# Optimization experiments

Measured on AMD Instinct MI355X. Metric: run time of the kernel, lower is better.

## Reference

```python
import jax, jax.numpy as jnp
import numpy as np

H = 32

def setup_inputs() -> dict:
    key = jax.random.key(0)
    ks = jax.random.split(key, 8)
    B, S = 256, 4096
    scale = 1.0 / np.sqrt(H)
    return {
        "lstm_outputs": jax.random.normal(ks[0], (B, S, H), dtype=jnp.float32),
        "final_hidden": jax.random.normal(ks[1], (B, H), dtype=jnp.float32),
        "Wq": jax.random.uniform(ks[2], (H, H), jnp.float32, -scale, scale),
        "bq": jax.random.uniform(ks[3], (H,), jnp.float32, -scale, scale),
        "Wk": jax.random.uniform(ks[4], (H, H), jnp.float32, -scale, scale),
        "bk": jax.random.uniform(ks[5], (H,), jnp.float32, -scale, scale),
        "Wv": jax.random.uniform(ks[6], (H, 1), jnp.float32, -scale, scale),
        "bv": jax.random.uniform(ks[7], (1,), jnp.float32, -scale, scale),
    }

def reference(lstm_outputs, final_hidden, Wq, bq, Wk, bk, Wv, bv):
    # keys: [B,S,H], query: [B,H]
    keys = jnp.einsum('bsh,hd->bsd', lstm_outputs, Wk) + bk
    query = final_hidden @ Wq + bq
    tanhed = jnp.tanh(query[:, None, :] + keys)            # [B,S,H]
    scores = jnp.einsum('bsh,h->bs', tanhed, Wv[:, 0]) + bv[0]  # [B,S]
    att_weights = jax.nn.softmax(scores, axis=-1)          # [B,S]
    context = jnp.einsum('bs,bsh->bh', att_weights, keys)  # [B,H]
    return context, att_weights
```

## Files before the change

kernel.cpp:

```cpp
#include <hip/hip_runtime.h>
#include <math.h>

#define HD 32
#define BB 256
#define SS 4096
#define CHUNK 512
#define NC (SS / CHUNK)
#define BLK 256
#define PART_STRIDE 34

__device__ __forceinline__ float tanh_fast(float x) {
  float e = __builtin_amdgcn_exp2f(x * 2.8853900817779268f);
  return 1.0f - 2.0f * __builtin_amdgcn_rcpf(e + 1.0f);
}
__device__ __forceinline__ float exp_fast(float x) {
  return __builtin_amdgcn_exp2f(x * 1.4426950408889634f);
}

__global__ void __launch_bounds__(BLK) bahdanau_p1(
    const float* __restrict__ lstm, const float* __restrict__ fh,
    const float* __restrict__ Wq, const float* __restrict__ bq,
    const float* __restrict__ Wk, const float* __restrict__ bk,
    const float* __restrict__ Wv, const float* __restrict__ bv,
    float* __restrict__ scores_out, float* __restrict__ partials) {
  __shared__ float sWk[HD * HD];
  __shared__ float sQ[HD];
  __shared__ float sWv[HD];
  __shared__ float sBk[HD];
  __shared__ float sRedM[BLK / 64];
  __shared__ float sRedL[BLK / 64];
  __shared__ float sRedC[BLK / 64][HD];

  const int tid = threadIdx.x;
  const int b = blockIdx.x / NC;
  const int chunk = blockIdx.x % NC;
  const int base = chunk * CHUNK;

  ((float4*)sWk)[tid] = ((const float4*)Wk)[tid];
  if (tid < HD) {
    sWv[tid] = Wv[tid];
    sBk[tid] = bk[tid];
    float acc = bq[tid];
    const float* fhb = fh + b * HD;
#pragma unroll
    for (int j = 0; j < HD; j++) acc += fhb[j] * Wq[j * HD + tid];
    sQ[tid] = acc;
  }
  __syncthreads();

  const int sA = base + tid;
  const int sB = sA + BLK;
  const float* rowA = lstm + ((size_t)b * SS + sA) * HD;
  const float* rowB = rowA + (size_t)BLK * HD;

  float4 xA[8], xB[8];
#pragma unroll
  for (int q = 0; q < 8; q++) {
    xA[q] = ((const float4*)rowA)[q];
    xB[q] = ((const float4*)rowB)[q];
  }

  float keyA[HD], keyB[HD];
#pragma unroll
  for (int q = 0; q < 8; q++) {
    float4 b4 = ((const float4*)sBk)[q];
    keyA[4 * q + 0] = b4.x; keyA[4 * q + 1] = b4.y;
    keyA[4 * q + 2] = b4.z; keyA[4 * q + 3] = b4.w;
    keyB[4 * q + 0] = b4.x; keyB[4 * q + 1] = b4.y;
    keyB[4 * q + 2] = b4.z; keyB[4 * q + 3] = b4.w;
  }

#pragma unroll
  for (int jq = 0; jq < 8; jq++) {
    const float a4[4] = {xA[jq].x, xA[jq].y, xA[jq].z, xA[jq].w};
    const float c4[4] = {xB[jq].x, xB[jq].y, xB[jq].z, xB[jq].w};
#pragma unroll
    for (int jj = 0; jj < 4; jj++) {
      const float aj = a4[jj];
      const float cj = c4[jj];
      const float* wrow = sWk + (jq * 4 + jj) * HD;
#pragma unroll
      for (int hq = 0; hq < 8; hq++) {
        float4 w = ((const float4*)wrow)[hq];
        keyA[4 * hq + 0] += aj * w.x; keyA[4 * hq + 1] += aj * w.y;
        keyA[4 * hq + 2] += aj * w.z; keyA[4 * hq + 3] += aj * w.w;
        keyB[4 * hq + 0] += cj * w.x; keyB[4 * hq + 1] += cj * w.y;
        keyB[4 * hq + 2] += cj * w.z; keyB[4 * hq + 3] += cj * w.w;
      }
    }
  }

  const float bv0 = bv[0];
  float scA = bv0, scB = bv0;
#pragma unroll
  for (int h = 0; h < HD; h++) {
    const float q = sQ[h], wv = sWv[h];
    scA += tanh_fast(q + keyA[h]) * wv;
    scB += tanh_fast(q + keyB[h]) * wv;
  }
  scores_out[(size_t)b * SS + sA] = scA;
  scores_out[(size_t)b * SS + sB] = scB;

  const int wid = tid >> 6, lane = tid & 63;
  float m = fmaxf(scA, scB);
#pragma unroll
  for (int off = 32; off >= 1; off >>= 1) m = fmaxf(m, __shfl_xor(m, off, 64));
  if (lane == 0) sRedM[wid] = m;
  __syncthreads();
  m = fmaxf(fmaxf(sRedM[0], sRedM[1]), fmaxf(sRedM[2], sRedM[3]));

  const float eA = exp_fast(scA - m);
  const float eB = exp_fast(scB - m);
  float l = eA + eB;
#pragma unroll
  for (int off = 32; off >= 1; off >>= 1) l += __shfl_xor(l, off, 64);
  if (lane == 0) sRedL[wid] = l;

#pragma unroll
  for (int h = 0; h < HD; h++) {
    float v = eA * keyA[h] + eB * keyB[h];
#pragma unroll
    for (int off = 32; off >= 1; off >>= 1) v += __shfl_xor(v, off, 64);
    if (lane == 0) sRedC[wid][h] = v;
  }
  __syncthreads();

  if (tid < HD) {
    float c = sRedC[0][tid] + sRedC[1][tid] + sRedC[2][tid] + sRedC[3][tid];
    float* p = partials + (size_t)(b * NC + chunk) * PART_STRIDE;
    p[2 + tid] = c;
    if (tid == 0) {
      p[0] = m;
      p[1] = sRedL[0] + sRedL[1] + sRedL[2] + sRedL[3];
    }
  }
}

__global__ void __launch_bounds__(BLK) bahdanau_p2(
    const float* __restrict__ partials, float* __restrict__ ctx_out,
    float* __restrict__ scores) {
  const int b = blockIdx.x;
  const int tid = threadIdx.x;
  __shared__ float sM, sInvL;
  __shared__ float sAl[NC];

  if (tid == 0) {
    float m = -1e30f;
    for (int c = 0; c < NC; c++)
      m = fmaxf(m, partials[(size_t)(b * NC + c) * PART_STRIDE]);
    float L = 0.f;
    for (int c = 0; c < NC; c++) {
      const float* p = partials + (size_t)(b * NC + c) * PART_STRIDE;
      float a = exp_fast(p[0] - m);
      sAl[c] = a;
      L += a * p[1];
    }
    sM = m;
    sInvL = __builtin_amdgcn_rcpf(L);
  }
  __syncthreads();
  const float m = sM, invL = sInvL;

  if (tid < HD) {
    float c = 0.f;
#pragma unroll
    for (int cc = 0; cc < NC; cc++)
      c += sAl[cc] * partials[(size_t)(b * NC + cc) * PART_STRIDE + 2 + tid];
    ctx_out[b * HD + tid] = c * invL;
  }

  float* srow = scores + (size_t)b * SS;
  for (int s = tid; s < SS; s += BLK) {
    srow[s] = exp_fast(srow[s] - m) * invL;
  }
}

extern "C" void kernel_launch(void* const* d_in, const int* in_sizes, int n_in,
                              void* d_out, int out_size, void* d_ws,
                              size_t ws_size, hipStream_t stream) {
  const float* lstm = (const float*)d_in[0];
  const float* fh   = (const float*)d_in[1];
  const float* Wq   = (const float*)d_in[2];
  const float* bq   = (const float*)d_in[3];
  const float* Wk   = (const float*)d_in[4];
  const float* bk   = (const float*)d_in[5];
  const float* Wv   = (const float*)d_in[6];
  const float* bv   = (const float*)d_in[7];

  float* out = (float*)d_out;
  float* ctx_out = out;
  float* scores = out + BB * HD;
  float* partials = (float*)d_ws;

  bahdanau_p1<<<BB * NC, BLK, 0, stream>>>(lstm, fh, Wq, bq, Wk, bk, Wv, bv,
                                           scores, partials);
  bahdanau_p2<<<BB, BLK, 0, stream>>>(partials, ctx_out, scores);
}
```

Before: 249.3 us.

## Read Wk via uniform scalar loads, hoist row loads, split normalize kernel per chunk

```diff
diff --git a/kernel.cpp b/kernel.cpp
--- a/kernel.cpp
+++ b/kernel.cpp
@@ -9,6 +9,8 @@
 #define BLK 256
 #define PART_STRIDE 34
 
+typedef float vf32 __attribute__((ext_vector_type(32)));
+
 __device__ __forceinline__ float tanh_fast(float x) {
   float e = __builtin_amdgcn_exp2f(x * 2.8853900817779268f);
   return 1.0f - 2.0f * __builtin_amdgcn_rcpf(e + 1.0f);
@@ -17,16 +19,13 @@
   return __builtin_amdgcn_exp2f(x * 1.4426950408889634f);
 }
 
-__global__ void __launch_bounds__(BLK) bahdanau_p1(
+__global__ void __launch_bounds__(BLK, 3) bahdanau_p1(
     const float* __restrict__ lstm, const float* __restrict__ fh,
     const float* __restrict__ Wq, const float* __restrict__ bq,
     const float* __restrict__ Wk, const float* __restrict__ bk,
     const float* __restrict__ Wv, const float* __restrict__ bv,
     float* __restrict__ scores_out, float* __restrict__ partials) {
-  __shared__ float sWk[HD * HD];
   __shared__ float sQ[HD];
-  __shared__ float sWv[HD];
-  __shared__ float sBk[HD];
   __shared__ float sRedM[BLK / 64];
   __shared__ float sRedL[BLK / 64];
   __shared__ float sRedC[BLK / 64][HD];
@@ -36,10 +35,26 @@
   const int chunk = blockIdx.x % NC;
   const int base = chunk * CHUNK;
 
-  ((float4*)sWk)[tid] = ((const float4*)Wk)[tid];
+  const int sA = base + tid;
+  const int sB = sA + BLK;
+  const float* rowA = lstm + ((size_t)b * SS + sA) * HD;
+  const float* rowB = rowA + (size_t)BLK * HD;
+
+  vf32 xA, xB;
+#pragma unroll
+  for (int q = 0; q < 8; q++) {
+    float4 t = ((const float4*)rowA)[q];
+    xA[4 * q + 0] = t.x; xA[4 * q + 1] = t.y;
+    xA[4 * q + 2] = t.z; xA[4 * q + 3] = t.w;
+  }
+#pragma unroll
+  for (int q = 0; q < 8; q++) {
+    float4 t = ((const float4*)rowB)[q];
+    xB[4 * q + 0] = t.x; xB[4 * q + 1] = t.y;
+    xB[4 * q + 2] = t.z; xB[4 * q + 3] = t.w;
+  }
+
   if (tid < HD) {
-    sWv[tid] = Wv[tid];
-    sBk[tid] = bk[tid];
     float acc = bq[tid];
     const float* fhb = fh + b * HD;
 #pragma unroll
@@ -48,45 +63,21 @@
   }
   __syncthreads();
 
-  const int sA = base + tid;
-  const int sB = sA + BLK;
-  const float* rowA = lstm + ((size_t)b * SS + sA) * HD;
-  const float* rowB = rowA + (size_t)BLK * HD;
-
-  float4 xA[8], xB[8];
+  vf32 kA, kB;
 #pragma unroll
-  for (int q = 0; q < 8; q++) {
-    xA[q] = ((const float4*)rowA)[q];
-    xB[q] = ((const float4*)rowB)[q];
+  for (int h = 0; h < HD; h++) {
+    float bkh = bk[h];
+    kA[h] = bkh; kB[h] = bkh;
   }
-
-  float keyA[HD], keyB[HD];
 #pragma unroll
-  for (int q = 0; q < 8; q++) {
-    float4 b4 = ((const float4*)sBk)[q];
-    keyA[4 * q + 0] = b4.x; keyA[4 * q + 1] = b4.y;
-    keyA[4 * q + 2] = b4.z; keyA[4 * q + 3] = b4.w;
-    keyB[4 * q + 0] = b4.x; keyB[4 * q + 1] = b4.y;
-    keyB[4 * q + 2] = b4.z; keyB[4 * q + 3] = b4.w;
-  }
-
+  for (int j = 0; j < HD; j++) {
+    const float xa = xA[j];
+    const float xb = xB[j];
 #pragma unroll
-  for (int jq = 0; jq < 8; jq++) {
-    const float a4[4] = {xA[jq].x, xA[jq].y, xA[jq].z, xA[jq].w};
-    const float c4[4] = {xB[jq].x, xB[jq].y, xB[jq].z, xB[jq].w};
-#pragma unroll
-    for (int jj = 0; jj < 4; jj++) {
-      const float aj = a4[jj];
-      const float cj = c4[jj];
-      const float* wrow = sWk + (jq * 4 + jj) * HD;
-#pragma unroll
-      for (int hq = 0; hq < 8; hq++) {
-        float4 w = ((const float4*)wrow)[hq];
-        keyA[4 * hq + 0] += aj * w.x; keyA[4 * hq + 1] += aj * w.y;
-        keyA[4 * hq + 2] += aj * w.z; keyA[4 * hq + 3] += aj * w.w;
-        keyB[4 * hq + 0] += cj * w.x; keyB[4 * hq + 1] += cj * w.y;
-        keyB[4 * hq + 2] += cj * w.z; keyB[4 * hq + 3] += cj * w.w;
-      }
+    for (int h = 0; h < HD; h++) {
+      const float w = Wk[j * HD + h];
+      kA[h] = fmaf(xa, w, kA[h]);
+      kB[h] = fmaf(xb, w, kB[h]);
     }
   }
 
@@ -94,9 +85,10 @@
   float scA = bv0, scB = bv0;
 #pragma unroll
   for (int h = 0; h < HD; h++) {
-    const float q = sQ[h], wv = sWv[h];
-    scA += tanh_fast(q + keyA[h]) * wv;
-    scB += tanh_fast(q + keyB[h]) * wv;
+    const float qh = sQ[h];
+    const float wv = Wv[h];
+    scA = fmaf(tanh_fast(qh + kA[h]), wv, scA);
+    scB = fmaf(tanh_fast(qh + kB[h]), wv, scB);
   }
   scores_out[(size_t)b * SS + sA] = scA;
   scores_out[(size_t)b * SS + sB] = scB;
@@ -118,7 +110,7 @@
 
 #pragma unroll
   for (int h = 0; h < HD; h++) {
-    float v = eA * keyA[h] + eB * keyB[h];
+    float v = fmaf(eA, kA[h], eB * kB[h]);
 #pragma unroll
     for (int off = 32; off >= 1; off >>= 1) v += __shfl_xor(v, off, 64);
     if (lane == 0) sRedC[wid][h] = v;
@@ -139,40 +131,38 @@
 __global__ void __launch_bounds__(BLK) bahdanau_p2(
     const float* __restrict__ partials, float* __restrict__ ctx_out,
     float* __restrict__ scores) {
-  const int b = blockIdx.x;
+  const int b = blockIdx.x / NC;
+  const int chunk = blockIdx.x % NC;
   const int tid = threadIdx.x;
-  __shared__ float sM, sInvL;
-  __shared__ float sAl[NC];
 
-  if (tid == 0) {
-    float m = -1e30f;
-    for (int c = 0; c < NC; c++)
-      m = fmaxf(m, partials[(size_t)(b * NC + c) * PART_STRIDE]);
-    float L = 0.f;
-    for (int c = 0; c < NC; c++) {
-      const float* p = partials + (size_t)(b * NC + c) * PART_STRIDE;
-      float a = exp_fast(p[0] - m);
-      sAl[c] = a;
-      L += a * p[1];
-    }
-    sM = m;
-    sInvL = __builtin_amdgcn_rcpf(L);
+  float m = -1e30f;
+#pragma unroll
+  for (int c = 0; c < NC; c++)
+    m = fmaxf(m, partials[(size_t)(b * NC + c) * PART_STRIDE]);
+  float L = 0.f;
+  float al[NC];
+#pragma unroll
+  for (int c = 0; c < NC; c++) {
+    const float* p = partials + (size_t)(b * NC + c) * PART_STRIDE;
+    float a = exp_fast(p[0] - m);
+    al[c] = a;
+    L = fmaf(a, p[1], L);
   }
-  __syncthreads();
-  const float m = sM, invL = sInvL;
+  const float invL = __builtin_amdgcn_rcpf(L);
 
-  if (tid < HD) {
+  if (chunk == 0 && tid < HD) {
     float c = 0.f;
 #pragma unroll
     for (int cc = 0; cc < NC; cc++)
-      c += sAl[cc] * partials[(size_t)(b * NC + cc) * PART_STRIDE + 2 + tid];
+      c += al[cc] * partials[(size_t)(b * NC + cc) * PART_STRIDE + 2 + tid];
     ctx_out[b * HD + tid] = c * invL;
   }
 
-  float* srow = scores + (size_t)b * SS;
-  for (int s = tid; s < SS; s += BLK) {
-    srow[s] = exp_fast(srow[s] - m) * invL;
-  }
+  float2* srow = (float2*)(scores + (size_t)b * SS + chunk * CHUNK);
+  float2 s = srow[tid];
+  s.x = exp_fast(s.x - m) * invL;
+  s.y = exp_fast(s.y - m) * invL;
+  srow[tid] = s;
 }
 
 extern "C" void kernel_launch(void* const* d_in, const int* in_sizes, int n_in,
@@ -194,5 +184,5 @@
 
   bahdanau_p1<<<BB * NC, BLK, 0, stream>>>(lstm, fh, Wq, bq, Wk, bk, Wv, bv,
                                            scores, partials);
-  bahdanau_p2<<<BB, BLK, 0, stream>>>(partials, ctx_out, scores);
+  bahdanau_p2<<<BB * NC, BLK, 0, stream>>>(partials, ctx_out, scores);
 }
```

Result: faster. 239.2 us (-4.1%).
